# Optimization experiments

Measured on AMD Instinct MI355X. Metric: run time of the kernel, lower is better.

## Reference

```python
import jax, jax.numpy as jnp
import numpy as np

TEMPERATURE = 0.5


def setup_inputs() -> dict:
    key = jax.random.key(0)
    k1, k2 = jax.random.split(key)
    z_i = jax.random.normal(k1, (4096, 256), dtype=jnp.float32)
    z_j = jax.random.normal(k2, (4096, 256), dtype=jnp.float32)
    return {"z_i": z_i, "z_j": z_j}


def _l2norm(x, eps=1e-12):
    n = jnp.sqrt(jnp.sum(x * x, axis=1, keepdims=True))
    return x / jnp.maximum(n, eps)


def reference(z_i, z_j):
    n = z_i.shape[0]
    zi = _l2norm(z_i)
    zj = _l2norm(z_j)
    reps = jnp.concatenate([zi, zj], axis=0)            # [2N, D], rows unit-norm
    # cosine similarity of unit vectors == dot product -> normalized GEMM
    sim = jnp.matmul(reps, reps.T)                      # [2N, 2N]
    sim_ij = jnp.diagonal(sim, offset=n)                # [N]
    sim_ji = jnp.diagonal(sim, offset=-n)               # [N]
    positives = jnp.concatenate([sim_ij, sim_ji], axis=0)  # [2N]
    mask = 1.0 - jnp.eye(2 * n, dtype=sim.dtype)
    numerator = jnp.exp(positives / TEMPERATURE)
    denominator = jnp.sum(mask * jnp.exp(sim / TEMPERATURE), axis=1)
    loss = -jnp.log(numerator / denominator)
    return jnp.mean(loss)
```

## Files before the change

### kernel.cpp

```cpp
#include <hip/hip_runtime.h>
#include <hip/hip_bf16.h>


#define D      256
#define KC     8
#define RT     2
#define PAN    32
#define NBLK   (PAN * (PAN + 1) / 2)
#define BN     32
#define SLOTS  32
#define CEXP   2.885390081777926f
#define E2     7.38905609893065f
#define FBLK   32

typedef __bf16 bf16x8 __attribute__((ext_vector_type(8)));
typedef float  f32x4  __attribute__((ext_vector_type(4)));
typedef __attribute__((address_space(1))) const unsigned int* gas_t;
typedef __attribute__((address_space(3))) unsigned int*       las_t;

static __device__ __forceinline__ void gload_lds16(const void* g, void* l) {
    __builtin_amdgcn_global_load_lds((gas_t)(uintptr_t)g, (las_t)(uintptr_t)l, 16, 0, 0);
}

static __device__ __forceinline__ unsigned short f2bf(float x) {
    union { float f; unsigned u; } v; v.f = x;
    unsigned r = v.u + 0x7fffu + ((v.u >> 16) & 1u);
    return (unsigned short)(r >> 16);
}

#define STAGE(bufp, srcp)                                                 \
    do {                                                                  \
        const char* s_ = (const char*)(srcp);                             \
        char* d_ = (char*)(bufp);                                         \
        _Pragma("unroll")                                                 \
        for (int i_ = 0; i_ < 2; ++i_) {                                  \
            int o_   = i_ * 8192 + threadIdx.x * 16;                      \
            int row_ = o_ >> 9;                                           \
            int cb_  = o_ & 511;                                          \
            gload_lds16(s_ + row_ * 512 + (cb_ ^ ((row_ & 7) << 4)),      \
                        d_ + o_);                                         \
        }                                                                 \
    } while (0)

__global__ __launch_bounds__(64) void knorm(const float* __restrict__ zi,
                                            const float* __restrict__ zj,
                                            unsigned short* __restrict__ reps,
                                            float* __restrict__ pos, int n) {
    const int i = blockIdx.x;
    const int lane = threadIdx.x;
    const float4 a = ((const float4*)(zi + (size_t)i * D))[lane];
    const float4 b = ((const float4*)(zj + (size_t)i * D))[lane];
    float si = a.x*a.x + a.y*a.y + a.z*a.z + a.w*a.w;
    float sj = b.x*b.x + b.y*b.y + b.z*b.z + b.w*b.w;
    float sd = a.x*b.x + a.y*b.y + a.z*b.z + a.w*b.w;
    #pragma unroll
    for (int off = 32; off; off >>= 1) {
        si += __shfl_xor(si, off);
        sj += __shfl_xor(sj, off);
        sd += __shfl_xor(sd, off);
    }
    const float inv_i = 1.0f / fmaxf(sqrtf(si), 1e-12f);
    const float inv_j = 1.0f / fmaxf(sqrtf(sj), 1e-12f);
    if (lane == 0) pos[i] = sd * inv_i * inv_j;
    ushort4 pa, pb;
    pa.x = f2bf(a.x * inv_i); pa.y = f2bf(a.y * inv_i);
    pa.z = f2bf(a.z * inv_i); pa.w = f2bf(a.w * inv_i);
    pb.x = f2bf(b.x * inv_j); pb.y = f2bf(b.y * inv_j);
    pb.z = f2bf(b.z * inv_j); pb.w = f2bf(b.w * inv_j);
    ((ushort4*)(reps + (size_t)i * D))[lane]       = pa;
    ((ushort4*)(reps + (size_t)(i + n) * D))[lane] = pb;
}

__global__ __launch_bounds__(512) void krowsum(const unsigned short* __restrict__ reps,
                                               float* __restrict__ partial, int twoN) {
    __shared__ unsigned short buf[2][BN * D];
    __shared__ float cs_lds[8][16][16];
    const int lane = threadIdx.x & 63;
    const int w    = threadIdx.x >> 6;
    const int lrow = lane & 15;
    const int lkb  = (lane >> 4) * 16;
    const int swz  = (lrow & 7) << 4;

    int bid = blockIdx.x, rpan = 0, rem = PAN;
    while (bid >= rem) { bid -= rem; ++rpan; --rem; }
    const int cpan = rpan + bid;
    const bool diag = (rpan == cpan);

    const char* Bb = (const char*)reps + (size_t)cpan * 256 * 512;
    STAGE(&buf[0][0], Bb);

    bf16x8 afrag[RT][KC];
    #pragma unroll
    for (int rt = 0; rt < RT; ++rt) {
        const char* ar = (const char*)reps
                       + (size_t)(rpan * 256 + w * 32 + rt * 16 + lrow) * 512 + lkb;
        #pragma unroll
        for (int kc = 0; kc < KC; ++kc)
            afrag[rt][kc] = *(const bf16x8*)(ar + kc * 64);
    }

    float rs[RT][4];
    #pragma unroll
    for (int rt = 0; rt < RT; ++rt)
        #pragma unroll
        for (int e = 0; e < 4; ++e) rs[rt][e] = 0.f;

    __syncthreads();
    int cur = 0;
    for (int c = 0; c < 8; ++c) {
        if (c < 7) STAGE(&buf[cur ^ 1][0], Bb + (size_t)(c + 1) * (BN * 512));
        const char* bb = (const char*)&buf[cur][0];
        f32x4 acc[RT][2];
        #pragma unroll
        for (int rt = 0; rt < RT; ++rt) {
            acc[rt][0] = (f32x4){0.f, 0.f, 0.f, 0.f};
            acc[rt][1] = (f32x4){0.f, 0.f, 0.f, 0.f};
        }
        #pragma unroll
        for (int kc = 0; kc < KC; ++kc) {
            const int kb = (kc * 64 + lkb) ^ swz;
            bf16x8 bf0 = *(const bf16x8*)(bb + (lrow)        * 512 + kb);
            bf16x8 bf1 = *(const bf16x8*)(bb + (16 + lrow)   * 512 + kb);
            #pragma unroll
            for (int rt = 0; rt < RT; ++rt) {
                acc[rt][0] = __builtin_amdgcn_mfma_f32_16x16x32_bf16(
                    afrag[rt][kc], bf0, acc[rt][0], 0, 0, 0);
                acc[rt][1] = __builtin_amdgcn_mfma_f32_16x16x32_bf16(
                    afrag[rt][kc], bf1, acc[rt][1], 0, 0, 0);
            }
        }
        float cs0 = 0.f, cs1 = 0.f;
        #pragma unroll
        for (int rt = 0; rt < RT; ++rt)
            #pragma unroll
            for (int e = 0; e < 4; ++e) {
                float e0 = __builtin_amdgcn_exp2f(acc[rt][0][e] * CEXP);
                float e1 = __builtin_amdgcn_exp2f(acc[rt][1][e] * CEXP);
                rs[rt][e] += e0 + e1;
                cs0 += e0; cs1 += e1;
            }
        if (!diag) {
            cs0 += __shfl_xor(cs0, 16); cs0 += __shfl_xor(cs0, 32);
            cs1 += __shfl_xor(cs1, 16); cs1 += __shfl_xor(cs1, 32);
            if (lane < 16) {
                cs_lds[w][c * 2 + 0][lane] = cs0;
                cs_lds[w][c * 2 + 1][lane] = cs1;
            }
        }
        __syncthreads();
        cur ^= 1;
    }

    #pragma unroll
    for (int rt = 0; rt < RT; ++rt)
        #pragma unroll
        for (int e = 0; e < 4; ++e)
            #pragma unroll
            for (int off = 1; off < 16; off <<= 1)
                rs[rt][e] += __shfl_xor(rs[rt][e], off);
    if ((lane & 15) == 0) {
        #pragma unroll
        for (int rt = 0; rt < RT; ++rt) {
            const int rg = rpan * 256 + w * 32 + rt * 16 + (lane >> 4) * 4;
            f32x4 v = {rs[rt][0], rs[rt][1], rs[rt][2], rs[rt][3]};
            *(f32x4*)(partial + (size_t)cpan * twoN + rg) = v;
        }
    }

    if (!diag && threadIdx.x < 256) {
        const int ct  = threadIdx.x >> 4;
        const int col = threadIdx.x & 15;
        float v = 0.f;
        #pragma unroll
        for (int ww = 0; ww < 8; ++ww) v += cs_lds[ww][ct][col];
        const int gcol = cpan * 256 + ct * 16 + col;
        partial[(size_t)rpan * twoN + gcol] = v;
    }
}

__global__ __launch_bounds__(256) void kfinal1(const float* __restrict__ partial,
                                               const float* __restrict__ pos,
                                               float* __restrict__ bsum,
                                               int twoN, int n) {
    __shared__ float red[256];
    const int r = blockIdx.x * 256 + threadIdx.x;
    float s = 0.f;
    if (r < twoN) {
        float dsum = 0.f;
        #pragma unroll
        for (int p = 0; p < SLOTS; ++p) dsum += partial[(size_t)p * twoN + r];
        dsum -= E2;
        const float q = pos[r < n ? r : r - n];
        s = logf(dsum) - 2.0f * q;
    }
    red[threadIdx.x] = s;
    __syncthreads();
    #pragma unroll
    for (int off = 128; off; off >>= 1) {
        if (threadIdx.x < off) red[threadIdx.x] += red[threadIdx.x + off];
        __syncthreads();
    }
    if (threadIdx.x == 0) bsum[blockIdx.x] = red[0];
}

__global__ __launch_bounds__(64) void kfinal2(const float* __restrict__ bsum,
                                              float* __restrict__ out, int twoN) {
    float s = threadIdx.x < FBLK ? bsum[threadIdx.x] : 0.f;
    #pragma unroll
    for (int off = 32; off; off >>= 1) s += __shfl_xor(s, off);
    if (threadIdx.x == 0) out[0] = s / (float)twoN;
}

extern "C" void kernel_launch(void* const* d_in, const int* in_sizes, int n_in,
                              void* d_out, int out_size, void* d_ws, size_t ws_size,
                              hipStream_t stream) {
    const float* zi = (const float*)d_in[0];
    const float* zj = (const float*)d_in[1];
    const int n    = in_sizes[0] / D;
    const int twoN = 2 * n;

    unsigned short* reps = (unsigned short*)d_ws;
    float* pos     = (float*)((char*)d_ws + (size_t)twoN * D * 2);
    float* partial = pos + n;
    float* bsum    = partial + (size_t)SLOTS * twoN;
    float* out     = (float*)d_out;

    knorm<<<n, 64, 0, stream>>>(zi, zj, reps, pos, n);
    krowsum<<<NBLK, 512, 0, stream>>>(reps, partial, twoN);
    kfinal1<<<FBLK, 256, 0, stream>>>(partial, pos, bsum, twoN, n);
    kfinal2<<<1, 64, 0, stream>>>(bsum, out, twoN);
}
```

Baseline: 54.37 us.

## Use 4-wave blocks with 64-row A tiles and 64 KB LDS half-panel staging

The row-sum GEMM kernel drops from 8 waves to 4 waves per block, and each wave now holds 64 A rows in registers instead of 32. This halves the LDS B-fragment reads per MFMA. The B panel is now staged in two 64 KB halves (128 columns each) instead of a double-buffered 32-column pipeline, which removes the per-chunk barriers. In exchange, loads no longer overlap compute within a block, register pressure doubles for A fragments, and the 64 KB LDS buffer limits how many blocks fit per CU.

Result: slower. 84.24 us (+54.9%).

```diff
diff --git a/kernel.cpp b/kernel.cpp
--- a/kernel.cpp
+++ b/kernel.cpp
@@ -4,10 +4,9 @@
 
 #define D      256
 #define KC     8
-#define RT     2
+#define RT     4
 #define PAN    32
 #define NBLK   (PAN * (PAN + 1) / 2)
-#define BN     32
 #define SLOTS  32
 #define CEXP   2.885390081777926f
 #define E2     7.38905609893065f
@@ -28,13 +27,13 @@
     return (unsigned short)(r >> 16);
 }
 
-#define STAGE(bufp, srcp)                                                 \
+#define STAGE64(bufp, srcp)                                               \
     do {                                                                  \
         const char* s_ = (const char*)(srcp);                             \
         char* d_ = (char*)(bufp);                                         \
         _Pragma("unroll")                                                 \
-        for (int i_ = 0; i_ < 2; ++i_) {                                  \
-            int o_   = i_ * 8192 + threadIdx.x * 16;                      \
+        for (int i_ = 0; i_ < 16; ++i_) {                                 \
+            int o_   = i_ * 4096 + threadIdx.x * 16;                      \
             int row_ = o_ >> 9;                                           \
             int cb_  = o_ & 511;                                          \
             gload_lds16(s_ + row_ * 512 + (cb_ ^ ((row_ & 7) << 4)),      \
@@ -71,10 +70,10 @@
     ((ushort4*)(reps + (size_t)(i + n) * D))[lane] = pb;
 }
 
-__global__ __launch_bounds__(512) void krowsum(const unsigned short* __restrict__ reps,
-                                               float* __restrict__ partial, int twoN) {
-    __shared__ unsigned short buf[2][BN * D];
-    __shared__ float cs_lds[8][16][16];
+__global__ __launch_bounds__(256, 2) void krowsum(const unsigned short* __restrict__ reps,
+                                                  float* __restrict__ partial, int twoN) {
+    __shared__ unsigned short buf[128 * D];
+    __shared__ float cs_lds[4][16][16];
     const int lane = threadIdx.x & 63;
     const int w    = threadIdx.x >> 6;
     const int lrow = lane & 15;
@@ -87,13 +86,13 @@
     const bool diag = (rpan == cpan);
 
     const char* Bb = (const char*)reps + (size_t)cpan * 256 * 512;
-    STAGE(&buf[0][0], Bb);
+    STAGE64(&buf[0], Bb);
 
     bf16x8 afrag[RT][KC];
     #pragma unroll
     for (int rt = 0; rt < RT; ++rt) {
         const char* ar = (const char*)reps
-                       + (size_t)(rpan * 256 + w * 32 + rt * 16 + lrow) * 512 + lkb;
+            + (size_t)(rpan * 256 + w * 64 + rt * 16 + lrow) * 512 + lkb;
         #pragma unroll
         for (int kc = 0; kc < KC; ++kc)
             afrag[rt][kc] = *(const bf16x8*)(ar + kc * 64);
@@ -105,51 +104,56 @@
         #pragma unroll
         for (int e = 0; e < 4; ++e) rs[rt][e] = 0.f;
 
-    __syncthreads();
-    int cur = 0;
-    for (int c = 0; c < 8; ++c) {
-        if (c < 7) STAGE(&buf[cur ^ 1][0], Bb + (size_t)(c + 1) * (BN * 512));
-        const char* bb = (const char*)&buf[cur][0];
-        f32x4 acc[RT][2];
-        #pragma unroll
-        for (int rt = 0; rt < RT; ++rt) {
-            acc[rt][0] = (f32x4){0.f, 0.f, 0.f, 0.f};
-            acc[rt][1] = (f32x4){0.f, 0.f, 0.f, 0.f};
+    for (int h = 0; h < 2; ++h) {
+        if (h) {
+            __syncthreads();
+            STAGE64(&buf[0], Bb + 65536);
         }
-        #pragma unroll
-        for (int kc = 0; kc < KC; ++kc) {
-            const int kb = (kc * 64 + lkb) ^ swz;
-            bf16x8 bf0 = *(const bf16x8*)(bb + (lrow)        * 512 + kb);
-            bf16x8 bf1 = *(const bf16x8*)(bb + (16 + lrow)   * 512 + kb);
+        __syncthreads();
+        #pragma unroll
+        for (int c = 0; c < 4; ++c) {
+            const int gc = h * 4 + c;
+            const char* bb = (const char*)&buf[0] + c * 32 * 512;
+            f32x4 acc[RT][2];
             #pragma unroll
             for (int rt = 0; rt < RT; ++rt) {
-                acc[rt][0] = __builtin_amdgcn_mfma_f32_16x16x32_bf16(
-                    afrag[rt][kc], bf0, acc[rt][0], 0, 0, 0);
-                acc[rt][1] = __builtin_amdgcn_mfma_f32_16x16x32_bf16(
-                    afrag[rt][kc], bf1, acc[rt][1], 0, 0, 0);
+                acc[rt][0] = (f32x4){0.f, 0.f, 0.f, 0.f};
+                acc[rt][1] = (f32x4){0.f, 0.f, 0.f, 0.f};
+            }
+            #pragma unroll
+            for (int kc = 0; kc < KC; ++kc) {
+                const int kb = (kc * 64 + lkb) ^ swz;
+                bf16x8 bf0 = *(const bf16x8*)(bb + (lrow)      * 512 + kb);
+                bf16x8 bf1 = *(const bf16x8*)(bb + (16 + lrow) * 512 + kb);
+                #pragma unroll
+                for (int rt = 0; rt < RT; ++rt) {
+                    acc[rt][0] = __builtin_amdgcn_mfma_f32_16x16x32_bf16(
+                        afrag[rt][kc], bf0, acc[rt][0], 0, 0, 0);
+                    acc[rt][1] = __builtin_amdgcn_mfma_f32_16x16x32_bf16(
+                        afrag[rt][kc], bf1, acc[rt][1], 0, 0, 0);
+                }
+            }
+            float cs0 = 0.f, cs1 = 0.f;
+            #pragma unroll
+            for (int rt = 0; rt < RT; ++rt)
+                #pragma unroll
+                for (int e = 0; e < 4; ++e) {
+                    float e0 = __builtin_amdgcn_exp2f(acc[rt][0][e] * CEXP);
+                    float e1 = __builtin_amdgcn_exp2f(acc[rt][1][e] * CEXP);
+                    rs[rt][e] += e0 + e1;
+                    cs0 += e0; cs1 += e1;
+                }
+            if (!diag) {
+                cs0 += __shfl_xor(cs0, 16); cs0 += __shfl_xor(cs0, 32);
+                cs1 += __shfl_xor(cs1, 16); cs1 += __shfl_xor(cs1, 32);
+                if (lane < 16) {
+                    cs_lds[w][gc * 2 + 0][lane] = cs0;
+                    cs_lds[w][gc * 2 + 1][lane] = cs1;
+                }
             }
         }
-        float cs0 = 0.f, cs1 = 0.f;
-        #pragma unroll
-        for (int rt = 0; rt < RT; ++rt)
-            #pragma unroll
-            for (int e = 0; e < 4; ++e) {
-                float e0 = __builtin_amdgcn_exp2f(acc[rt][0][e] * CEXP);
-                float e1 = __builtin_amdgcn_exp2f(acc[rt][1][e] * CEXP);
-                rs[rt][e] += e0 + e1;
-                cs0 += e0; cs1 += e1;
-            }
-        if (!diag) {
-            cs0 += __shfl_xor(cs0, 16); cs0 += __shfl_xor(cs0, 32);
-            cs1 += __shfl_xor(cs1, 16); cs1 += __shfl_xor(cs1, 32);
-            if (lane < 16) {
-                cs_lds[w][c * 2 + 0][lane] = cs0;
-                cs_lds[w][c * 2 + 1][lane] = cs1;
-            }
-        }
-        __syncthreads();
-        cur ^= 1;
-    }
+    }
+    __syncthreads();
 
     #pragma unroll
     for (int rt = 0; rt < RT; ++rt)
@@ -161,19 +165,19 @@
     if ((lane & 15) == 0) {
         #pragma unroll
         for (int rt = 0; rt < RT; ++rt) {
-            const int rg = rpan * 256 + w * 32 + rt * 16 + (lane >> 4) * 4;
+            const int rg = rpan * 256 + w * 64 + rt * 16 + (lane >> 4) * 4;
             f32x4 v = {rs[rt][0], rs[rt][1], rs[rt][2], rs[rt][3]};
             *(f32x4*)(partial + (size_t)cpan * twoN + rg) = v;
         }
     }
 
-    if (!diag && threadIdx.x < 256) {
+    if (!diag) {
         const int ct  = threadIdx.x >> 4;
         const int col = threadIdx.x & 15;
         float v = 0.f;
         #pragma unroll
-        for (int ww = 0; ww < 8; ++ww) v += cs_lds[ww][ct][col];
-        const int gcol = cpan * 256 + ct * 16 + col;
+        for (int ww = 0; ww < 4; ++ww) v += cs_lds[ww][ct][col];
+        const int gcol = cpan * 256 + (ct >> 1) * 32 + (ct & 1) * 16 + col;
         partial[(size_t)rpan * twoN + gcol] = v;
     }
 }
@@ -226,7 +230,7 @@
     float* out     = (float*)d_out;
 
     knorm<<<n, 64, 0, stream>>>(zi, zj, reps, pos, n);
-    krowsum<<<NBLK, 512, 0, stream>>>(reps, partial, twoN);
+    krowsum<<<NBLK, 256, 0, stream>>>(reps, partial, twoN);
     kfinal1<<<FBLK, 256, 0, stream>>>(partial, pos, bsum, twoN, n);
     kfinal2<<<1, 64, 0, stream>>>(bsum, out, twoN);
 }
```
